# Performance work log

Hardware: AMD Instinct MI355X
Metric: run time of the kernel (lower is better)

## Reference

```python
import jax, jax.numpy as jnp
import numpy as np

D_MODEL = 128
N_HEADS = 8
HEAD_DIM = D_MODEL // N_HEADS
N_NODES = 50000
N_EDGES = 640000


def setup_inputs() -> dict:
    key = jax.random.key(0)
    ks = jax.random.split(key, 10)
    sd = 1.0 / np.sqrt(D_MODEL)
    return {
        "node_embeds": jax.random.normal(ks[0], (N_NODES, D_MODEL), dtype=jnp.float32),
        "edge_index": jax.random.randint(ks[1], (2, N_EDGES), 0, N_NODES, dtype=jnp.int64),
        "Wq": jax.random.uniform(ks[2], (D_MODEL, D_MODEL), jnp.float32, -sd, sd),
        "bq": jax.random.uniform(ks[3], (D_MODEL,), jnp.float32, -sd, sd),
        "Wk": jax.random.uniform(ks[4], (D_MODEL, D_MODEL), jnp.float32, -sd, sd),
        "bk": jax.random.uniform(ks[5], (D_MODEL,), jnp.float32, -sd, sd),
        "Wv": jax.random.uniform(ks[6], (D_MODEL, D_MODEL), jnp.float32, -sd, sd),
        "bv": jax.random.uniform(ks[7], (D_MODEL,), jnp.float32, -sd, sd),
        "gamma": jnp.ones((D_MODEL,), jnp.float32),
        "beta": jnp.zeros((D_MODEL,), jnp.float32),
    }


def reference(node_embeds, edge_index, Wq, bq, Wk, bk, Wv, bv, gamma, beta):
    num_nodes = node_embeds.shape[0]
    rows, cols = edge_index[0], edge_index[1]
    src = node_embeds[rows]  # (E, d)
    tgt = node_embeds[cols]  # (E, d)
    q = (src @ Wq.T + bq).reshape(-1, N_HEADS, HEAD_DIM)
    k = (tgt @ Wk.T + bk).reshape(-1, N_HEADS, HEAD_DIM)
    v = (tgt @ Wv.T + bv).reshape(-1, N_HEADS, HEAD_DIM)
    att = jnp.einsum('ehd,ehd->eh', q, k) / jnp.sqrt(jnp.float32(HEAD_DIM))
    exp_att = jnp.exp(jnp.clip(att, -10.0, 10.0))  # (E, h)
    att_sum = jax.ops.segment_sum(exp_att, rows, num_segments=num_nodes)  # (N, h)
    att_norm = exp_att / (att_sum[rows] + 1e-8)
    weighted_v = (att_norm[..., None] * v).reshape(-1, D_MODEL)  # (E, d)
    out = jax.ops.segment_sum(weighted_v, rows, num_segments=num_nodes)
    out = out + node_embeds
    # LayerNorm, eps=1e-6
    mu = jnp.mean(out, axis=-1, keepdims=True)
    var = jnp.mean(jnp.square(out - mu), axis=-1, keepdims=True)
    out = (out - mu) * jax.lax.rsqrt(var + 1e-6) * gamma + beta
    return out
```

## Files before the change

### kernel.cpp

```cpp
#include <hip/hip_runtime.h>
#include <hip/hip_bf16.h>
#include <cstdint>

#define D_MODEL 128
#define N_HEADS 8
#define HEAD_DIM 16

typedef __attribute__((ext_vector_type(8))) short bf16x8;
typedef __attribute__((ext_vector_type(4))) float f32x4;

static __device__ __forceinline__ float b2f(unsigned short u) {
  unsigned int x = ((unsigned int)u) << 16;
  return __builtin_bit_cast(float, x);
}
static __device__ __forceinline__ unsigned short f2b(float f) {
  __hip_bfloat16 h = __float2bfloat16(f);
  return __builtin_bit_cast(unsigned short, h);
}

__global__ __launch_bounds__(256) void hist_cvtw_kernel(
    const int* __restrict__ rows, int* __restrict__ cnt, int E,
    const float* __restrict__ Wq, const float* __restrict__ Wk,
    const float* __restrict__ Wv, unsigned short* __restrict__ Wb)
{
  if (blockIdx.x < 24) {
    const int wb = blockIdx.x;
    const int m  = wb >> 3;
    const float* src = (m == 0) ? Wq : (m == 1) ? Wk : Wv;
    unsigned short* dst = Wb + (size_t)m * 16384;
    const int base = ((wb & 7) * 256 + threadIdx.x) * 8;
    const float4 a = reinterpret_cast<const float4*>(src + base)[0];
    const float4 c = reinterpret_cast<const float4*>(src + base)[1];
    unsigned short tmp[8];
    tmp[0] = f2b(a.x); tmp[1] = f2b(a.y); tmp[2] = f2b(a.z); tmp[3] = f2b(a.w);
    tmp[4] = f2b(c.x); tmp[5] = f2b(c.y); tmp[6] = f2b(c.z); tmp[7] = f2b(c.w);
    reinterpret_cast<uint4*>(dst + base)[0] = *reinterpret_cast<uint4*>(tmp);
  } else {
    const int e = (blockIdx.x - 24) * 256 + threadIdx.x;
    if (e < E) atomicAdd(&cnt[rows[e]], 1);
  }
}

__global__ __launch_bounds__(256) void partial_kernel(
    const int* __restrict__ cnt, int* __restrict__ bsum, int N)
{
  __shared__ int wsum[4];
  const int t = threadIdx.x;
  const int base = blockIdx.x * 1024 + t * 4;
  int s = 0;
  #pragma unroll
  for (int i = 0; i < 4; ++i)
    if (base + i < N) s += cnt[base + i];
  #pragma unroll
  for (int off = 32; off > 0; off >>= 1) s += __shfl_xor(s, off, 64);
  if ((t & 63) == 0) wsum[t >> 6] = s;
  __syncthreads();
  if (t == 0) bsum[blockIdx.x] = wsum[0] + wsum[1] + wsum[2] + wsum[3];
}

__global__ __launch_bounds__(256) void scansums_kernel(
    const int* __restrict__ bsum, int* __restrict__ boff, int nb)
{
  __shared__ int p[256];
  __shared__ int carry_s;
  const int t = threadIdx.x;
  if (t == 0) carry_s = 0;
  __syncthreads();
  for (int c0 = 0; c0 < nb; c0 += 256) {
    const int v = (c0 + t < nb) ? bsum[c0 + t] : 0;
    p[t] = v;
    __syncthreads();
    for (int off = 1; off < 256; off <<= 1) {
      const int other = (t >= off) ? p[t - off] : 0;
      __syncthreads();
      p[t] += other;
      __syncthreads();
    }
    const int carry = carry_s;
    if (c0 + t < nb) boff[c0 + t] = carry + p[t] - v;
    __syncthreads();
    if (t == 0) carry_s = carry + p[255];
    __syncthreads();
  }
}

__global__ __launch_bounds__(256) void emit_kernel(
    const int* __restrict__ cnt, const int* __restrict__ boff,
    int* __restrict__ row_ptr, int* __restrict__ row_cur, int N, int E)
{
  __shared__ int psum[256];
  const int t = threadIdx.x;
  const int base = blockIdx.x * 1024 + t * 4;
  int v[4];
  #pragma unroll
  for (int i = 0; i < 4; ++i)
    v[i] = (base + i < N) ? cnt[base + i] : 0;
  const int local = v[0] + v[1] + v[2] + v[3];
  psum[t] = local;
  __syncthreads();
  for (int off = 1; off < 256; off <<= 1) {
    const int other = (t >= off) ? psum[t - off] : 0;
    __syncthreads();
    psum[t] += other;
    __syncthreads();
  }
  int pre = boff[blockIdx.x] + psum[t] - local;
  #pragma unroll
  for (int i = 0; i < 4; ++i) {
    const int idx = base + i;
    if (idx < N) {
      row_ptr[idx] = pre;
      row_cur[idx] = pre;
      pre += v[i];
    }
  }
  if (blockIdx.x == 0 && t == 0) row_ptr[N] = E;
}

__global__ __launch_bounds__(256) void scatter_qkv_kernel(
    const int* __restrict__ rows, const int* __restrict__ cols,
    int* __restrict__ row_cur, int* __restrict__ csr_cols, int E,
    const float* __restrict__ X, const unsigned short* __restrict__ Wb,
    const float* __restrict__ bq, const float* __restrict__ bk,
    const float* __restrict__ bv,
    unsigned short* __restrict__ Qo, unsigned short* __restrict__ Ko,
    unsigned short* __restrict__ Vo, int N, int nbQ)
{
  __shared__ unsigned short Wl[128 * 128];

  if ((int)blockIdx.x >= nbQ) {
    const int e = (blockIdx.x - nbQ) * 256 + threadIdx.x;
    if (e < E) {
      const int pos = atomicAdd(&row_cur[rows[e]], 1);
      csr_cols[pos] = cols[e];
    }
    return;
  }

  const int t    = threadIdx.x;
  const int wave = t >> 6;
  const int l    = t & 63;
  const int lr   = l & 15;
  const int lg   = l >> 4;
  const int nw   = blockIdx.x * 128 + wave * 32;

  bf16x8 a[2][4];
  #pragma unroll
  for (int ng = 0; ng < 2; ++ng) {
    const int arow = nw + ng * 16 + lr;
    if (arow < N) {
      const float* xp = X + (size_t)arow * D_MODEL + lg * 8;
      #pragma unroll
      for (int ks = 0; ks < 4; ++ks) {
        const float4 f0 = reinterpret_cast<const float4*>(xp + ks * 32)[0];
        const float4 f1 = reinterpret_cast<const float4*>(xp + ks * 32)[1];
        unsigned short tm[8];
        tm[0] = f2b(f0.x); tm[1] = f2b(f0.y); tm[2] = f2b(f0.z); tm[3] = f2b(f0.w);
        tm[4] = f2b(f1.x); tm[5] = f2b(f1.y); tm[6] = f2b(f1.z); tm[7] = f2b(f1.w);
        a[ng][ks] = *reinterpret_cast<bf16x8*>(tm);
      }
    } else {
      #pragma unroll
      for (int ks = 0; ks < 4; ++ks) a[ng][ks] = bf16x8{0,0,0,0,0,0,0,0};
    }
  }

  const float* biases[3] = {bq, bk, bv};
  unsigned short* outs[3] = {Qo, Ko, Vo};

  #pragma unroll 1
  for (int m = 0; m < 3; ++m) {
    __syncthreads();
    {
      const uint4* wsrc = reinterpret_cast<const uint4*>(Wb + (size_t)m * 16384);
      uint4* wl4 = reinterpret_cast<uint4*>(Wl);
      #pragma unroll
      for (int i = 0; i < 8; ++i) {
        const int cg = i * 256 + t;
        const int r  = cg >> 4;
        const int j  = cg & 15;
        wl4[r * 16 + (j ^ (r & 7))] = wsrc[cg];
      }
    }
    __syncthreads();

    unsigned short* __restrict__ O = outs[m];
    const float* __restrict__ bias = biases[m];
    float bias8[8];
    #pragma unroll
    for (int c = 0; c < 8; ++c) bias8[c] = bias[c * 16 + lr];

    #pragma unroll
    for (int c = 0; c < 8; ++c) {
      const int row = c * 16 + lr;
      bf16x8 w[4];
      #pragma unroll
      for (int ks = 0; ks < 4; ++ks) {
        const int j = ks * 4 + lg;
        w[ks] = *reinterpret_cast<const bf16x8*>(
            Wl + ((row * 16 + (j ^ (row & 7))) * 8));
      }
      #pragma unroll
      for (int ng = 0; ng < 2; ++ng) {
        f32x4 acc = {bias8[c], bias8[c], bias8[c], bias8[c]};
        #pragma unroll
        for (int ks = 0; ks < 4; ++ks)
          acc = __builtin_amdgcn_mfma_f32_16x16x32_bf16(a[ng][ks], w[ks], acc, 0, 0, 0);
        #pragma unroll
        for (int r = 0; r < 4; ++r) {
          const int orow = nw + ng * 16 + lg * 4 + r;
          if (orow < N) O[(size_t)orow * D_MODEL + c * 16 + lr] = f2b(acc[r]);
        }
      }
    }
  }
}

__global__ __launch_bounds__(256) void fused_kernel(
    const unsigned short* __restrict__ Q, const unsigned short* __restrict__ K,
    const unsigned short* __restrict__ V, const float* __restrict__ X,
    const int* __restrict__ row_ptr, const int* __restrict__ csr_cols,
    const float* __restrict__ gamma, const float* __restrict__ beta,
    float* __restrict__ out, int N)
{
  __shared__ float lds[4][576];
  const int wv = threadIdx.x >> 6;
  const int n  = blockIdx.x * 4 + wv;
  if (n >= N) return;
  const int l  = threadIdx.x & 63;
  const int h  = l & 7;
  const int g  = l >> 3;
  const int hd = l >> 3;

  unsigned* __restrict__ Vu = reinterpret_cast<unsigned*>(lds[wv]);
  float*    __restrict__ El = lds[wv] + 512;

  float qf[16];
  {
    const unsigned short* qp = Q + (size_t)n * D_MODEL + h * HEAD_DIM;
    const bf16x8 q0 = *reinterpret_cast<const bf16x8*>(qp);
    const bf16x8 q1 = *reinterpret_cast<const bf16x8*>(qp + 8);
    #pragma unroll
    for (int i = 0; i < 8; ++i) {
      qf[i]     = b2f((unsigned short)q0[i]);
      qf[8 + i] = b2f((unsigned short)q1[i]);
    }
  }

  float accx = 0.f, accy = 0.f, dlane = 0.f;
  const int e0 = row_ptr[n];
  const int e1 = row_ptr[n + 1];

  const int rcol = (l & 7) * 64;
  const int rrot = (l >> 3) + 4 * (l & 7);

  for (int eb = e0; eb < e1; eb += 8) {
    const int  eg    = eb + g;
    const bool valid = eg < e1;
    const int  c     = valid ? csr_cols[eg] : 0;

    const unsigned short* kp = K + (size_t)c * D_MODEL + h * HEAD_DIM;
    const unsigned short* vp = V + (size_t)c * D_MODEL + h * HEAD_DIM;
    const bf16x8 k0 = *reinterpret_cast<const bf16x8*>(kp);
    const bf16x8 k1 = *reinterpret_cast<const bf16x8*>(kp + 8);
    const bf16x8 v0 = *reinterpret_cast<const bf16x8*>(vp);
    const bf16x8 v1 = *reinterpret_cast<const bf16x8*>(vp + 8);

    float s = 0.f;
    #pragma unroll
    for (int i = 0; i < 8; ++i) {
      s = fmaf(qf[i],     b2f((unsigned short)k0[i]), s);
      s = fmaf(qf[8 + i], b2f((unsigned short)k1[i]), s);
    }
    s *= 0.25f;
    s = fminf(fmaxf(s, -10.f), 10.f);
    const float ea = valid ? __expf(s) : 0.f;
    dlane += ea;

    El[l] = ea;
    {
      const uint4 u0 = __builtin_bit_cast(uint4, v0);
      const uint4 u1 = __builtin_bit_cast(uint4, v1);
      Vu[0 * 64 + ((l +  0) & 63)] = u0.x;
      Vu[1 * 64 + ((l +  4) & 63)] = u0.y;
      Vu[2 * 64 + ((l +  8) & 63)] = u0.z;
      Vu[3 * 64 + ((l + 12) & 63)] = u0.w;
      Vu[4 * 64 + ((l + 16) & 63)] = u1.x;
      Vu[5 * 64 + ((l + 20) & 63)] = u1.y;
      Vu[6 * 64 + ((l + 24) & 63)] = u1.z;
      Vu[7 * 64 + ((l + 28) & 63)] = u1.w;
    }
    __builtin_amdgcn_sched_barrier(0);

    #pragma unroll
    for (int j = 0; j < 8; ++j) {
      const float    aj = El[j * 8 + hd];
      const unsigned vv = Vu[rcol + ((j * 8 + rrot) & 63)];
      accx = fmaf(aj, b2f((unsigned short)(vv & 0xffffu)), accx);
      accy = fmaf(aj, b2f((unsigned short)(vv >> 16)), accy);
    }
    __builtin_amdgcn_sched_barrier(0);
  }

  dlane += __shfl_xor(dlane, 8,  64);
  dlane += __shfl_xor(dlane, 16, 64);
  dlane += __shfl_xor(dlane, 32, 64);
  const float denom = __shfl(dlane, hd, 64);

  const float inv = 1.f / (denom + 1e-8f);
  const float2 x = reinterpret_cast<const float2*>(X + (size_t)n * D_MODEL)[l];
  const float a0 = accx * inv + x.x;
  const float a1 = accy * inv + x.y;

  float sm = a0 + a1;
  float ss = a0 * a0 + a1 * a1;
  #pragma unroll
  for (int off = 32; off > 0; off >>= 1) {
    sm += __shfl_xor(sm, off, 64);
    ss += __shfl_xor(ss, off, 64);
  }
  const float mean = sm * (1.f / 128.f);
  const float var  = ss * (1.f / 128.f) - mean * mean;
  const float rs   = rsqrtf(var + 1e-6f);
  const float2 gm = reinterpret_cast<const float2*>(gamma)[l];
  const float2 bt = reinterpret_cast<const float2*>(beta)[l];
  float2 o;
  o.x = (a0 - mean) * rs * gm.x + bt.x;
  o.y = (a1 - mean) * rs * gm.y + bt.y;
  reinterpret_cast<float2*>(out + (size_t)n * D_MODEL)[l] = o;
}

extern "C" void kernel_launch(void* const* d_in, const int* in_sizes, int n_in,
                              void* d_out, int out_size, void* d_ws, size_t ws_size,
                              hipStream_t stream)
{
  const float* X     = (const float*)d_in[0];
  const int*   ei    = (const int*)  d_in[1];
  const float* Wq    = (const float*)d_in[2];
  const float* bq    = (const float*)d_in[3];
  const float* Wk    = (const float*)d_in[4];
  const float* bk    = (const float*)d_in[5];
  const float* Wv    = (const float*)d_in[6];
  const float* bv    = (const float*)d_in[7];
  const float* gamma = (const float*)d_in[8];
  const float* beta  = (const float*)d_in[9];

  const int N = in_sizes[0] / D_MODEL;
  const int E = in_sizes[1] / 2;
  const int* rows = ei;
  const int* cols = ei + E;

  const size_t nd = (size_t)N * D_MODEL;
  unsigned short* Wb = (unsigned short*)d_ws;
  unsigned short* Qb = Wb + 3 * 16384;
  unsigned short* Kb = Qb + nd;
  unsigned short* Vb = Kb + nd;
  int* row_cnt  = (int*)(Vb + nd);
  int* row_ptr  = row_cnt + N;
  int* row_cur  = row_ptr + N + 1;
  int* csr_cols = row_cur + N;
  int* bsum     = csr_cols + E;
  int* boff     = bsum + ((N + 1023) / 1024) + 1;

  const int nb  = (N + 1023) / 1024;
  const int nbE = (E + 255) / 256;
  const int nbQ = (N + 127) / 128;

  hipMemsetAsync(row_cnt, 0, (size_t)N * sizeof(int), stream);

  hist_cvtw_kernel<<<24 + nbE, 256, 0, stream>>>(
      rows, row_cnt, E, Wq, Wk, Wv, Wb);

  partial_kernel<<<nb, 256, 0, stream>>>(row_cnt, bsum, N);
  scansums_kernel<<<1, 256, 0, stream>>>(bsum, boff, nb);
  emit_kernel<<<nb, 256, 0, stream>>>(row_cnt, boff, row_ptr, row_cur, N, E);

  scatter_qkv_kernel<<<nbQ + nbE, 256, 0, stream>>>(
      rows, cols, row_cur, csr_cols, E,
      X, Wb, bq, bk, bv, Qb, Kb, Vb, N, nbQ);

  fused_kernel<<<(N + 3) / 4, 256, 0, stream>>>(
      Qb, Kb, Vb, X, row_ptr, csr_cols, gamma, beta, (float*)d_out, N);
}
```

Before: 140.8 us.

## Merge weight conversion into QKV kernel and collapse three-kernel scan into one

Each QKV block now converts the fp32 weights to bf16 itself while staging them into LDS, so the separate weight-conversion pass goes away. The histogram moves into the QKV launch. The partial-sum, single-block scan and emit kernels become one emit kernel in which each block re-reduces all preceding counts to find its offset. The CSR scatter becomes its own launch after emit. Launch count drops from six kernels to four, at the cost of redundant prefix reads (quadratic in block count, but small at this N) and repeated weight conversion in every QKV block.

New measurement: 149.3 us. 1.06x slower.

```diff
diff --git a/kernel.cpp b/kernel.cpp
--- a/kernel.cpp
+++ b/kernel.cpp
@@ -18,109 +18,11 @@
   return __builtin_bit_cast(unsigned short, h);
 }
 
-__global__ __launch_bounds__(256) void hist_cvtw_kernel(
+__global__ __launch_bounds__(256) void hist_qkv_kernel(
     const int* __restrict__ rows, int* __restrict__ cnt, int E,
+    const float* __restrict__ X,
     const float* __restrict__ Wq, const float* __restrict__ Wk,
-    const float* __restrict__ Wv, unsigned short* __restrict__ Wb)
-{
-  if (blockIdx.x < 24) {
-    const int wb = blockIdx.x;
-    const int m  = wb >> 3;
-    const float* src = (m == 0) ? Wq : (m == 1) ? Wk : Wv;
-    unsigned short* dst = Wb + (size_t)m * 16384;
-    const int base = ((wb & 7) * 256 + threadIdx.x) * 8;
-    const float4 a = reinterpret_cast<const float4*>(src + base)[0];
-    const float4 c = reinterpret_cast<const float4*>(src + base)[1];
-    unsigned short tmp[8];
-    tmp[0] = f2b(a.x); tmp[1] = f2b(a.y); tmp[2] = f2b(a.z); tmp[3] = f2b(a.w);
-    tmp[4] = f2b(c.x); tmp[5] = f2b(c.y); tmp[6] = f2b(c.z); tmp[7] = f2b(c.w);
-    reinterpret_cast<uint4*>(dst + base)[0] = *reinterpret_cast<uint4*>(tmp);
-  } else {
-    const int e = (blockIdx.x - 24) * 256 + threadIdx.x;
-    if (e < E) atomicAdd(&cnt[rows[e]], 1);
-  }
-}
-
-__global__ __launch_bounds__(256) void partial_kernel(
-    const int* __restrict__ cnt, int* __restrict__ bsum, int N)
-{
-  __shared__ int wsum[4];
-  const int t = threadIdx.x;
-  const int base = blockIdx.x * 1024 + t * 4;
-  int s = 0;
-  #pragma unroll
-  for (int i = 0; i < 4; ++i)
-    if (base + i < N) s += cnt[base + i];
-  #pragma unroll
-  for (int off = 32; off > 0; off >>= 1) s += __shfl_xor(s, off, 64);
-  if ((t & 63) == 0) wsum[t >> 6] = s;
-  __syncthreads();
-  if (t == 0) bsum[blockIdx.x] = wsum[0] + wsum[1] + wsum[2] + wsum[3];
-}
-
-__global__ __launch_bounds__(256) void scansums_kernel(
-    const int* __restrict__ bsum, int* __restrict__ boff, int nb)
-{
-  __shared__ int p[256];
-  __shared__ int carry_s;
-  const int t = threadIdx.x;
-  if (t == 0) carry_s = 0;
-  __syncthreads();
-  for (int c0 = 0; c0 < nb; c0 += 256) {
-    const int v = (c0 + t < nb) ? bsum[c0 + t] : 0;
-    p[t] = v;
-    __syncthreads();
-    for (int off = 1; off < 256; off <<= 1) {
-      const int other = (t >= off) ? p[t - off] : 0;
-      __syncthreads();
-      p[t] += other;
-      __syncthreads();
-    }
-    const int carry = carry_s;
-    if (c0 + t < nb) boff[c0 + t] = carry + p[t] - v;
-    __syncthreads();
-    if (t == 0) carry_s = carry + p[255];
-    __syncthreads();
-  }
-}
-
-__global__ __launch_bounds__(256) void emit_kernel(
-    const int* __restrict__ cnt, const int* __restrict__ boff,
-    int* __restrict__ row_ptr, int* __restrict__ row_cur, int N, int E)
-{
-  __shared__ int psum[256];
-  const int t = threadIdx.x;
-  const int base = blockIdx.x * 1024 + t * 4;
-  int v[4];
-  #pragma unroll
-  for (int i = 0; i < 4; ++i)
-    v[i] = (base + i < N) ? cnt[base + i] : 0;
-  const int local = v[0] + v[1] + v[2] + v[3];
-  psum[t] = local;
-  __syncthreads();
-  for (int off = 1; off < 256; off <<= 1) {
-    const int other = (t >= off) ? psum[t - off] : 0;
-    __syncthreads();
-    psum[t] += other;
-    __syncthreads();
-  }
-  int pre = boff[blockIdx.x] + psum[t] - local;
-  #pragma unroll
-  for (int i = 0; i < 4; ++i) {
-    const int idx = base + i;
-    if (idx < N) {
-      row_ptr[idx] = pre;
-      row_cur[idx] = pre;
-      pre += v[i];
-    }
-  }
-  if (blockIdx.x == 0 && t == 0) row_ptr[N] = E;
-}
-
-__global__ __launch_bounds__(256) void scatter_qkv_kernel(
-    const int* __restrict__ rows, const int* __restrict__ cols,
-    int* __restrict__ row_cur, int* __restrict__ csr_cols, int E,
-    const float* __restrict__ X, const unsigned short* __restrict__ Wb,
+    const float* __restrict__ Wv,
     const float* __restrict__ bq, const float* __restrict__ bk,
     const float* __restrict__ bv,
     unsigned short* __restrict__ Qo, unsigned short* __restrict__ Ko,
@@ -130,10 +32,7 @@
 
   if ((int)blockIdx.x >= nbQ) {
     const int e = (blockIdx.x - nbQ) * 256 + threadIdx.x;
-    if (e < E) {
-      const int pos = atomicAdd(&row_cur[rows[e]], 1);
-      csr_cols[pos] = cols[e];
-    }
+    if (e < E) atomicAdd(&cnt[rows[e]], 1);
     return;
   }
 
@@ -165,6 +64,7 @@
     }
   }
 
+  const float* wmats[3]  = {Wq, Wk, Wv};
   const float* biases[3] = {bq, bk, bv};
   unsigned short* outs[3] = {Qo, Ko, Vo};
 
@@ -172,14 +72,19 @@
   for (int m = 0; m < 3; ++m) {
     __syncthreads();
     {
-      const uint4* wsrc = reinterpret_cast<const uint4*>(Wb + (size_t)m * 16384);
+      const float* __restrict__ wsrc = wmats[m];
       uint4* wl4 = reinterpret_cast<uint4*>(Wl);
       #pragma unroll
       for (int i = 0; i < 8; ++i) {
         const int cg = i * 256 + t;
         const int r  = cg >> 4;
         const int j  = cg & 15;
-        wl4[r * 16 + (j ^ (r & 7))] = wsrc[cg];
+        const float4 f0 = reinterpret_cast<const float4*>(wsrc + cg * 8)[0];
+        const float4 f1 = reinterpret_cast<const float4*>(wsrc + cg * 8)[1];
+        unsigned short tm[8];
+        tm[0] = f2b(f0.x); tm[1] = f2b(f0.y); tm[2] = f2b(f0.z); tm[3] = f2b(f0.w);
+        tm[4] = f2b(f1.x); tm[5] = f2b(f1.y); tm[6] = f2b(f1.z); tm[7] = f2b(f1.w);
+        wl4[r * 16 + (j ^ (r & 7))] = *reinterpret_cast<uint4*>(tm);
       }
     }
     __syncthreads();
@@ -214,6 +119,68 @@
       }
     }
   }
+}
+
+__global__ __launch_bounds__(256) void emit_kernel(
+    const int* __restrict__ cnt, int* __restrict__ row_ptr,
+    int* __restrict__ row_cur, int N, int E)
+{
+  __shared__ int red[4];
+  __shared__ int psum[256];
+  __shared__ int base_s;
+  const int b = blockIdx.x;
+  const int t = threadIdx.x;
+
+  int s = 0;
+  {
+    const int npre4 = (b * 1024) >> 2;
+    const int4* c4 = reinterpret_cast<const int4*>(cnt);
+    for (int i = t; i < npre4; i += 256) {
+      const int4 v = c4[i];
+      s += v.x + v.y + v.z + v.w;
+    }
+  }
+  #pragma unroll
+  for (int off = 32; off > 0; off >>= 1) s += __shfl_xor(s, off, 64);
+  if ((t & 63) == 0) red[t >> 6] = s;
+  __syncthreads();
+  if (t == 0) base_s = red[0] + red[1] + red[2] + red[3];
+
+  const int base = b * 1024 + t * 4;
+  int v[4];
+  #pragma unroll
+  for (int i = 0; i < 4; ++i)
+    v[i] = (base + i < N) ? cnt[base + i] : 0;
+  const int local = v[0] + v[1] + v[2] + v[3];
+  psum[t] = local;
+  __syncthreads();
+  for (int off = 1; off < 256; off <<= 1) {
+    const int other = (t >= off) ? psum[t - off] : 0;
+    __syncthreads();
+    psum[t] += other;
+    __syncthreads();
+  }
+  int pre = base_s + psum[t] - local;
+  #pragma unroll
+  for (int i = 0; i < 4; ++i) {
+    const int idx = base + i;
+    if (idx < N) {
+      row_ptr[idx] = pre;
+      row_cur[idx] = pre;
+      pre += v[i];
+    }
+  }
+  if (b == 0 && t == 0) row_ptr[N] = E;
+}
+
+__global__ __launch_bounds__(256) void scatter_kernel(
+    const int* __restrict__ rows, const int* __restrict__ cols,
+    int* __restrict__ row_cur, int* __restrict__ csr_cols, int E)
+{
+  const int e = blockIdx.x * 256 + threadIdx.x;
+  if (e >= E) return;
+  const int pos = atomicAdd(&row_cur[rows[e]], 1);
+  csr_cols[pos] = cols[e];
 }
 
 __global__ __launch_bounds__(256) void fused_kernel(
@@ -351,16 +318,13 @@
   const int* cols = ei + E;
 
   const size_t nd = (size_t)N * D_MODEL;
-  unsigned short* Wb = (unsigned short*)d_ws;
-  unsigned short* Qb = Wb + 3 * 16384;
+  unsigned short* Qb = (unsigned short*)d_ws;
   unsigned short* Kb = Qb + nd;
   unsigned short* Vb = Kb + nd;
   int* row_cnt  = (int*)(Vb + nd);
   int* row_ptr  = row_cnt + N;
   int* row_cur  = row_ptr + N + 1;
   int* csr_cols = row_cur + N;
-  int* bsum     = csr_cols + E;
-  int* boff     = bsum + ((N + 1023) / 1024) + 1;
 
   const int nb  = (N + 1023) / 1024;
   const int nbE = (E + 255) / 256;
@@ -368,16 +332,12 @@
 
   hipMemsetAsync(row_cnt, 0, (size_t)N * sizeof(int), stream);
 
-  hist_cvtw_kernel<<<24 + nbE, 256, 0, stream>>>(
-      rows, row_cnt, E, Wq, Wk, Wv, Wb);
-
-  partial_kernel<<<nb, 256, 0, stream>>>(row_cnt, bsum, N);
-  scansums_kernel<<<1, 256, 0, stream>>>(bsum, boff, nb);
-  emit_kernel<<<nb, 256, 0, stream>>>(row_cnt, boff, row_ptr, row_cur, N, E);
-
-  scatter_qkv_kernel<<<nbQ + nbE, 256, 0, stream>>>(
-      rows, cols, row_cur, csr_cols, E,
-      X, Wb, bq, bk, bv, Qb, Kb, Vb, N, nbQ);
+  hist_qkv_kernel<<<nbQ + nbE, 256, 0, stream>>>(
+      rows, row_cnt, E, X, Wq, Wk, Wv, bq, bk, bv, Qb, Kb, Vb, N, nbQ);
+
+  emit_kernel<<<nb, 256, 0, stream>>>(row_cnt, row_ptr, row_cur, N, E);
+
+  scatter_kernel<<<nbE, 256, 0, stream>>>(rows, cols, row_cur, csr_cols, E);
 
   fused_kernel<<<(N + 3) / 4, 256, 0, stream>>>(
       Qb, Kb, Vb, X, row_ptr, csr_cols, gamma, beta, (float*)d_out, N);
```
